# Optimization experiments

Hardware: AMD Instinct MI355X
Metric: run time of the kernel (lower is better)

The kernel has to match this reference:

```python
import jax, jax.numpy as jnp
import numpy as np

T = 4096
HIDDEN = 2048
N_HEADS = 16
N_KV_HEADS = 4
HEAD_DIM = 128
WINDOW = 1024  # per_layer_sliding_window = WINDOW + 1 -> q attends keys with q_pos - k_pos <= WINDOW
ROPE_THETA = 100000.0
QKV_OUT = (N_HEADS + 2 * N_KV_HEADS) * HEAD_DIM  # 3072


def setup_inputs() -> dict:
    key = jax.random.key(0)
    k1, k2, k3, k4 = jax.random.split(key, 4)
    return {
        "hidden_states": jax.random.normal(k1, (T, HIDDEN), dtype=jnp.float32),
        "positions": jnp.arange(T, dtype=jnp.int32),
        "w_qkv": jax.random.normal(k2, (HIDDEN, QKV_OUT), dtype=jnp.float32) * 0.02,
        "b_qkv": jax.random.normal(k3, (QKV_OUT,), dtype=jnp.float32) * 0.02,
        "w_o": jax.random.normal(k4, (N_HEADS * HEAD_DIM, HIDDEN), dtype=jnp.float32) * 0.02,
    }


def _apply_rope(x, positions):
    # x: [T, n_heads, HEAD_DIM], neox-style rotary over full head dim
    half = HEAD_DIM // 2
    inv_freq = 1.0 / (ROPE_THETA ** (jnp.arange(half, dtype=jnp.float32) / half))
    freqs = positions.astype(jnp.float32)[:, None] * inv_freq[None, :]  # [T, half]
    cos = jnp.cos(freqs)[:, None, :]  # [T, 1, half]
    sin = jnp.sin(freqs)[:, None, :]
    x1, x2 = x[..., :half], x[..., half:]
    return jnp.concatenate([x1 * cos - x2 * sin, x2 * cos + x1 * sin], axis=-1)


def reference(hidden_states, positions, w_qkv, b_qkv, w_o):
    # QKV projection (bias=True)
    qkv = hidden_states @ w_qkv + b_qkv  # [T, QKV_OUT]
    q_size = N_HEADS * HEAD_DIM
    kv_size = N_KV_HEADS * HEAD_DIM
    q = qkv[:, :q_size].reshape(T, N_HEADS, HEAD_DIM)
    k = qkv[:, q_size:q_size + kv_size].reshape(T, N_KV_HEADS, HEAD_DIM)
    v = qkv[:, q_size + kv_size:].reshape(T, N_KV_HEADS, HEAD_DIM)

    # RoPE on q and k
    q = _apply_rope(q, positions)
    k = _apply_rope(k, positions)

    # GQA: expand kv heads to match query heads
    group = N_HEADS // N_KV_HEADS
    k = jnp.repeat(k, group, axis=1)  # [T, N_HEADS, HEAD_DIM]
    v = jnp.repeat(v, group, axis=1)

    scale = HEAD_DIM ** -0.5
    scores = jnp.einsum('qhd,khd->hqk', q, k) * scale  # [H, T, T]

    # causal + sliding-window mask: j <= i and i - j <= WINDOW
    i = jnp.arange(T)[:, None]
    j = jnp.arange(T)[None, :]
    mask = (j <= i) & (i - j <= WINDOW)  # [T, T]
    scores = jnp.where(mask[None, :, :], scores, jnp.finfo(scores.dtype).min)

    probs = jax.nn.softmax(scores, axis=-1)
    attn = jnp.einsum('hqk,khd->qhd', probs, v)  # [T, H, HEAD_DIM]
    attn = attn.reshape(T, N_HEADS * HEAD_DIM)

    # output projection (bias=False)
    return attn @ w_o
```

## Files before the change

### kernel.cpp

```cpp
#include <hip/hip_runtime.h>
#include <cstdint>

#define T_TOK 4096
#define HID 2048
#define NH 16
#define NKV 4
#define HD 128
#define WIN 1024
#define QKVO 3072

typedef float f32x4 __attribute__((ext_vector_type(4)));
typedef __bf16 bf16x8 __attribute__((ext_vector_type(8)));
typedef __bf16 bf16x4 __attribute__((ext_vector_type(4)));
typedef __bf16 bf16x2 __attribute__((ext_vector_type(2)));

__device__ __forceinline__ void gload16(const void* g, void* lds) {
  auto gp = reinterpret_cast<__attribute__((address_space(1))) void*>(
      reinterpret_cast<uintptr_t>(g));
  auto lp = reinterpret_cast<__attribute__((address_space(3))) void*>(
      reinterpret_cast<uintptr_t>(lds));
  __builtin_amdgcn_global_load_lds(gp, lp, 16, 0, 0);
}

__device__ __forceinline__ f32x4 mfma16(bf16x8 a, bf16x8 b, f32x4 c) {
  return __builtin_amdgcn_mfma_f32_16x16x32_bf16(a, b, c, 0, 0, 0);
}

__global__ __launch_bounds__(256) void k_f32_to_bf16(const float* __restrict__ x,
                                                     __bf16* __restrict__ y) {
  const size_t e = (size_t)blockIdx.x * 256 + threadIdx.x;
  const float4* xv = (const float4*)x;
  float4 a = xv[e * 2], b = xv[e * 2 + 1];
  bf16x8 o;
  o[0] = (__bf16)a.x; o[1] = (__bf16)a.y; o[2] = (__bf16)a.z; o[3] = (__bf16)a.w;
  o[4] = (__bf16)b.x; o[5] = (__bf16)b.y; o[6] = (__bf16)b.z; o[7] = (__bf16)b.w;
  *(bf16x8*)(y + e * 8) = o;
}

__global__ __launch_bounds__(256) void k_transpose(const float* __restrict__ W,
                                                   __bf16* __restrict__ Wt,
                                                   int R, int C) {
  __shared__ __bf16 tb[32][33];
  const int nbx = C >> 5;
  const int c0 = (blockIdx.x % nbx) << 5;
  const int r0 = (blockIdx.x / nbx) << 5;
  const int tx = threadIdx.x & 31, ty = threadIdx.x >> 5;
#pragma unroll
  for (int i = 0; i < 32; i += 8)
    tb[ty + i][tx] = (__bf16)W[(size_t)(r0 + ty + i) * C + c0 + tx];
  __syncthreads();
#pragma unroll
  for (int i = 0; i < 32; i += 8)
    Wt[(size_t)(c0 + ty + i) * R + r0 + tx] = tb[tx][ty + i];
}

__global__ void k_rope_tab(const int* __restrict__ pos, float* __restrict__ cosT,
                           float* __restrict__ sinT) {
  const int t = blockIdx.x;
  const int d = threadIdx.x;
  const float inv = exp2f(-(float)d * (16.609640474436812f / 64.0f));
  const float fr = (float)pos[t] * inv;
  cosT[t * 64 + d] = cosf(fr);
  sinT[t * 64 + d] = sinf(fr);
}

template <bool BIAS, typename OutT>
__global__ __launch_bounds__(256, 2) void k_gemm(const __bf16* __restrict__ A,
                                                 const __bf16* __restrict__ Bt,
                                                 const float* __restrict__ bias,
                                                 OutT* __restrict__ C,
                                                 int M, int N, int K) {
  __shared__ __align__(16) __bf16 As[128 * 32];
  __shared__ __align__(16) __bf16 Bs[128 * 32];
  const int tid = threadIdx.x;
  const int lane = tid & 63;
  const int w = tid >> 6;
  const int wr = w >> 1, wc = w & 1;
  const int c = lane & 15, g = lane >> 4;

  const int nbx = N >> 7;
  const int bx = blockIdx.x % nbx;
  const int by = blockIdx.x / nbx;
  const int m0 = by << 7, n0 = bx << 7;

  const int o0 = w * 2048 + lane * 16;
  const int r0 = o0 >> 6, cb0 = o0 & 63;
  const int o1 = o0 + 1024;
  const int r1 = o1 >> 6, cb1 = o1 & 63;
  const __bf16* gA0 = A + (size_t)(m0 + r0) * K + (cb0 >> 1);
  const __bf16* gA1 = A + (size_t)(m0 + r1) * K + (cb1 >> 1);
  const __bf16* gB0 = Bt + (size_t)(n0 + r0) * K + (cb0 >> 1);
  const __bf16* gB1 = Bt + (size_t)(n0 + r1) * K + (cb1 >> 1);
  char* lA0 = (char*)As + w * 2048;
  char* lA1 = lA0 + 1024;
  char* lB0 = (char*)Bs + w * 2048;
  char* lB1 = lB0 + 1024;

  f32x4 acc[4][4] = {};

  for (int kt = 0; kt < K; kt += 32) {
    __syncthreads();
    gload16(gA0 + kt, lA0);
    gload16(gA1 + kt, lA1);
    gload16(gB0 + kt, lB0);
    gload16(gB1 + kt, lB1);
    __syncthreads();
    bf16x8 af[4], bfr[4];
#pragma unroll
    for (int mi = 0; mi < 4; mi++)
      af[mi] = *(const bf16x8*)(As + ((wr * 64 + mi * 16 + c) * 32 + g * 8));
#pragma unroll
    for (int ni = 0; ni < 4; ni++)
      bfr[ni] = *(const bf16x8*)(Bs + ((wc * 64 + ni * 16 + c) * 32 + g * 8));
#pragma unroll
    for (int mi = 0; mi < 4; mi++)
#pragma unroll
      for (int ni = 0; ni < 4; ni++)
        acc[mi][ni] = mfma16(af[mi], bfr[ni], acc[mi][ni]);
  }

#pragma unroll
  for (int ni = 0; ni < 4; ni++) {
    const int col = n0 + wc * 64 + ni * 16 + c;
    const float bv = BIAS ? bias[col] : 0.0f;
#pragma unroll
    for (int mi = 0; mi < 4; mi++)
#pragma unroll
      for (int r = 0; r < 4; r++) {
        const int row = m0 + wr * 64 + mi * 16 + 4 * g + r;
        C[(size_t)row * N + col] = (OutT)(acc[mi][ni][r] + bv);
      }
  }
}

__global__ __launch_bounds__(256) void k_rope_pack(
    const __bf16* __restrict__ qkv, const float* __restrict__ cosT,
    const float* __restrict__ sinT, __bf16* __restrict__ Qp,
    __bf16* __restrict__ Kp, __bf16* __restrict__ Vt) {
  const int t0 = blockIdx.x * 64;
  const int hh = blockIdx.y;
  const int tid = threadIdx.x;
  const int col0 = hh * HD;
  __shared__ __bf16 lt[64][136];
  if (hh < NH + NKV) {
    const bool isq = hh < NH;
    const float s = isq ? 0.08838834764831845f : 1.0f;
    __bf16* base = isq ? (Qp + (size_t)hh * T_TOK * HD)
                       : (Kp + (size_t)(hh - NH) * T_TOK * HD);
#pragma unroll
    for (int jj = 0; jj < 2; jj++) {
      const int e = jj * 256 + tid;
      const int tl = e >> 3, ch = e & 7;
      const int tt = t0 + tl;
      const bf16x8 x1 = *(const bf16x8*)(qkv + (size_t)tt * QKVO + col0 + ch * 8);
      const bf16x8 x2 = *(const bf16x8*)(qkv + (size_t)tt * QKVO + col0 + 64 + ch * 8);
      const float4 c0 = *(const float4*)(cosT + tt * 64 + ch * 8);
      const float4 c1 = *(const float4*)(cosT + tt * 64 + ch * 8 + 4);
      const float4 s0 = *(const float4*)(sinT + tt * 64 + ch * 8);
      const float4 s1 = *(const float4*)(sinT + tt * 64 + ch * 8 + 4);
      const float cs[8] = {c0.x, c0.y, c0.z, c0.w, c1.x, c1.y, c1.z, c1.w};
      const float sn[8] = {s0.x, s0.y, s0.z, s0.w, s1.x, s1.y, s1.z, s1.w};
      bf16x8 o1, o2;
#pragma unroll
      for (int i = 0; i < 8; i++) {
        const float a = (float)x1[i], b = (float)x2[i];
        o1[i] = (__bf16)((a * cs[i] - b * sn[i]) * s);
        o2[i] = (__bf16)((b * cs[i] + a * sn[i]) * s);
      }
      const int d2s = isq ? ch * 8 : ((ch * 8) ^ ((tt & 7) << 3));
      __bf16* dst = base + (size_t)tt * HD;
      *(bf16x8*)(dst + d2s) = o1;
      *(bf16x8*)(dst + 64 + d2s) = o2;
    }
  } else {
    const int kv = hh - (NH + NKV);
#pragma unroll
    for (int jj = 0; jj < 4; jj++) {
      const int e = jj * 256 + tid;
      const int tl = e >> 4, dc = e & 15;
      *(bf16x8*)&lt[tl][dc * 8] =
          *(const bf16x8*)(qkv + (size_t)(t0 + tl) * QKVO + col0 + dc * 8);
    }
    __syncthreads();
#pragma unroll
    for (int jj = 0; jj < 32; jj++) {
      const int e = jj * 256 + tid;
      const int d = e >> 6, tl = e & 63;
      Vt[((size_t)kv * HD + d) * T_TOK + t0 + (tl ^ ((d & 7) << 3))] = lt[tl][d];
    }
  }
}

__global__ __launch_bounds__(512, 4) void k_attn(const __bf16* __restrict__ Qp,
                                                 const __bf16* __restrict__ Kp,
                                                 const __bf16* __restrict__ Vt,
                                                 __bf16* __restrict__ attnO) {
  __shared__ __align__(16) __bf16 Ks[2][64 * 128];
  __shared__ __align__(16) __bf16 Vs[2][128 * 64];
  __shared__ __align__(16) __bf16 Ps[8][16 * 64];

  const int tid = threadIdx.x;
  const int lane = tid & 63;
  const int w = tid >> 6;
  const int c = lane & 15, g = lane >> 4;
  const int h = blockIdx.y;
  const int kvh = h >> 2;
  const int qb = (int)(gridDim.x - 1) - (int)blockIdx.x;
  const int q0 = qb * 128;
  const int i_row = q0 + w * 16 + c;
  const int swz = (c & 7) << 4;

  bf16x8 qf[4];
  {
    const __bf16* qbase = Qp + ((size_t)h * T_TOK + i_row) * HD;
#pragma unroll
    for (int ds = 0; ds < 4; ds++) qf[ds] = *(const bf16x8*)(qbase + ds * 32 + g * 8);
  }

  f32x4 ot[8] = {};
  float mrun = 0.0f, lrun = 0.0f;

  const int jstart = (q0 >= WIN) ? (q0 - WIN) : 0;
  const int niter = (q0 + 128 - jstart) >> 6;

  const char* Kg = (const char*)Kp + (size_t)kvh * T_TOK * HD * 2;
  const char* Vg = (const char*)Vt + (size_t)kvh * HD * T_TOK * 2;
  const char* kg0 = Kg + (size_t)(jstart + 8 * w + (lane >> 4)) * 256 + (lane & 15) * 16;
  const char* vg0 = Vg + (size_t)(16 * w + (lane >> 3)) * (T_TOK * 2) +
                    (size_t)jstart * 2 + (lane & 7) * 16;

#pragma unroll
  for (int q = 0; q < 2; q++)
    gload16(kg0 + q * 1024, (char*)&Ks[0][0] + w * 2048 + q * 1024);
#pragma unroll
  for (int q = 0; q < 2; q++)
    gload16(vg0 + (size_t)q * 8 * (T_TOK * 2), (char*)&Vs[0][0] + w * 2048 + q * 1024);

  char* pw = (char*)&Ps[w][0];
  int cur = 0;

  for (int it = 0; it < niter; ++it) {
    const int j0 = jstart + it * 64;
    __syncthreads();

    if (it + 1 < niter) {
      const char* kg = kg0 + (size_t)(it + 1) * 16384;
      const char* vg = vg0 + (size_t)(it + 1) * 128;
      char* kd = (char*)&Ks[cur ^ 1][0] + w * 2048;
      char* vd = (char*)&Vs[cur ^ 1][0] + w * 2048;
#pragma unroll
      for (int q = 0; q < 2; q++) gload16(kg + q * 1024, kd + q * 1024);
#pragma unroll
      for (int q = 0; q < 2; q++)
        gload16(vg + (size_t)q * 8 * (T_TOK * 2), vd + q * 1024);
    }

    const char* kb = (const char*)&Ks[cur][0];
    const char* vb = (const char*)&Vs[cur][0];

    f32x4 st[4] = {};
    __builtin_amdgcn_s_setprio(1);
#pragma unroll
    for (int t = 0; t < 4; t++)
#pragma unroll
      for (int ds = 0; ds < 4; ds++) {
        bf16x8 kf = *(const bf16x8*)(kb + (t * 16 + c) * 256 + ((ds * 64 + g * 16) ^ swz));
        st[t] = mfma16(kf, qf[ds], st[t]);
      }
    __builtin_amdgcn_s_setprio(0);

    float p[16];
    float cmax = -1e30f;
    const int jb = i_row - j0 - 4 * g;
#pragma unroll
    for (int t = 0; t < 4; t++)
#pragma unroll
      for (int r = 0; r < 4; r++) {
        float s = st[t][r];
        s = ((unsigned)(jb - 16 * t - r) <= WIN) ? s : -1e30f;
        p[t * 4 + r] = s;
        cmax = fmaxf(cmax, s);
      }
    cmax = fmaxf(cmax, __shfl_xor(cmax, 16));
    cmax = fmaxf(cmax, __shfl_xor(cmax, 32));

    if (!__all(cmax <= mrun + 8.0f)) {
      const float mn = fmaxf(mrun, cmax);
      const float alpha = __expf(mrun - mn);
      lrun *= alpha;
#pragma unroll
      for (int m = 0; m < 8; m++) ot[m] *= alpha;
      mrun = mn;
    }
    float rs = 0.0f;
#pragma unroll
    for (int x = 0; x < 16; x++) {
      const float e_ = __expf(p[x] - mrun);
      p[x] = e_;
      rs += e_;
    }
    rs += __shfl_xor(rs, 16);
    rs += __shfl_xor(rs, 32);
    lrun += rs;

#pragma unroll
    for (int t = 0; t < 4; t++) {
      bf16x4 pk;
      pk[0] = (__bf16)p[t * 4 + 0];
      pk[1] = (__bf16)p[t * 4 + 1];
      pk[2] = (__bf16)p[t * 4 + 2];
      pk[3] = (__bf16)p[t * 4 + 3];
      *(bf16x4*)(pw + c * 128 + ((t * 32 + g * 8) ^ swz)) = pk;
    }
    bf16x8 pf[2];
#pragma unroll
    for (int ks = 0; ks < 2; ks++)
      pf[ks] = *(const bf16x8*)(pw + c * 128 + ((ks * 64 + g * 16) ^ swz));

    __builtin_amdgcn_s_setprio(1);
#pragma unroll
    for (int m = 0; m < 8; m++)
#pragma unroll
      for (int ks = 0; ks < 2; ks++) {
        bf16x8 vf = *(const bf16x8*)(vb + (m * 16 + c) * 128 + ((ks * 64 + g * 16) ^ swz));
        ot[m] = mfma16(vf, pf[ks], ot[m]);
      }
    __builtin_amdgcn_s_setprio(0);

    cur ^= 1;
  }

  const float inv_l = 1.0f / lrun;
  __bf16* orow = attnO + (size_t)i_row * (NH * HD) + h * HD;
#pragma unroll
  for (int m = 0; m < 8; m++) {
    bf16x4 o4;
#pragma unroll
    for (int r = 0; r < 4; r++) o4[r] = (__bf16)(ot[m][r] * inv_l);
    *(bf16x4*)(orow + m * 16 + 4 * g) = o4;
  }
}

extern "C" void kernel_launch(void* const* d_in, const int* in_sizes, int n_in,
                              void* d_out, int out_size, void* d_ws, size_t ws_size,
                              hipStream_t stream) {
  (void)in_sizes; (void)n_in; (void)out_size; (void)ws_size;
  const float* hidden = (const float*)d_in[0];
  const int* positions = (const int*)d_in[1];
  const float* w_qkv = (const float*)d_in[2];
  const float* b_qkv = (const float*)d_in[3];
  const float* w_o = (const float*)d_in[4];
  float* out = (float*)d_out;

  char* ws = (char*)d_ws;
  __bf16* Hb = (__bf16*)ws;    ws += (size_t)T_TOK * HID * 2;
  __bf16* Wqkvt = (__bf16*)ws; ws += (size_t)QKVO * HID * 2;
  __bf16* Wot = (__bf16*)ws;   ws += (size_t)HID * HID * 2;
  float* cosT = (float*)ws;    ws += (size_t)T_TOK * 64 * 4;
  float* sinT = (float*)ws;    ws += (size_t)T_TOK * 64 * 4;
  __bf16* qkv = (__bf16*)ws;   ws += (size_t)T_TOK * QKVO * 2;
  __bf16* Qp = (__bf16*)ws;    ws += (size_t)NH * T_TOK * HD * 2;
  __bf16* Kp = (__bf16*)ws;    ws += (size_t)NKV * T_TOK * HD * 2;
  __bf16* Vt = (__bf16*)ws;    ws += (size_t)NKV * HD * T_TOK * 2;
  __bf16* attnb = (__bf16*)ws; ws += (size_t)T_TOK * NH * HD * 2;

  k_f32_to_bf16<<<T_TOK * HID / (256 * 8), 256, 0, stream>>>(hidden, Hb);
  k_transpose<<<(QKVO / 32) * (HID / 32), 256, 0, stream>>>(w_qkv, Wqkvt, HID, QKVO);
  k_transpose<<<(HID / 32) * (HID / 32), 256, 0, stream>>>(w_o, Wot, HID, HID);
  k_rope_tab<<<T_TOK, 64, 0, stream>>>(positions, cosT, sinT);
  k_gemm<true, __bf16><<<(T_TOK / 128) * (QKVO / 128), 256, 0, stream>>>(
      Hb, Wqkvt, b_qkv, qkv, T_TOK, QKVO, HID);
  k_rope_pack<<<dim3(T_TOK / 64, NH + 2 * NKV), 256, 0, stream>>>(
      qkv, cosT, sinT, Qp, Kp, Vt);
  k_attn<<<dim3(T_TOK / 128, NH), 512, 0, stream>>>(Qp, Kp, Vt, attnb);
  k_gemm<false, float><<<(T_TOK / 128) * (HID / 128), 256, 0, stream>>>(
      attnb, Wot, nullptr, out, T_TOK, HID, HID);
}
```

Baseline: 199.4 us.

## Double-buffer GEMM LDS tiles, swizzle LDS layout, and remap blocks across XCDs

New measurement: 190.9 us. 1.04x faster.

```diff
diff --git a/kernel.cpp b/kernel.cpp
--- a/kernel.cpp
+++ b/kernel.cpp
@@ -70,53 +70,75 @@
                                                  const float* __restrict__ bias,
                                                  OutT* __restrict__ C,
                                                  int M, int N, int K) {
-  __shared__ __align__(16) __bf16 As[128 * 32];
-  __shared__ __align__(16) __bf16 Bs[128 * 32];
+  __shared__ __align__(16) __bf16 As[2][128 * 32];
+  __shared__ __align__(16) __bf16 Bs[2][128 * 32];
   const int tid = threadIdx.x;
   const int lane = tid & 63;
   const int w = tid >> 6;
   const int wr = w >> 1, wc = w & 1;
   const int c = lane & 15, g = lane >> 4;
-
-  const int nbx = N >> 7;
-  const int bx = blockIdx.x % nbx;
-  const int by = blockIdx.x / nbx;
+  const int gsw = g ^ ((c >> 1) & 3);
+
+  const int nstc = N >> 9;
+  const int bid = blockIdx.x;
+  const int xcd = bid & 7;
+  const int j = bid >> 3;
+  const int spx = (int)(gridDim.x >> 7);
+  const int s = xcd * spx + (j >> 4);
+  const int q = j & 15;
+  const int by = (s / nstc) * 4 + (q >> 2);
+  const int bx = (s % nstc) * 4 + (q & 3);
   const int m0 = by << 7, n0 = bx << 7;
 
   const int o0 = w * 2048 + lane * 16;
-  const int r0 = o0 >> 6, cb0 = o0 & 63;
+  const int r0 = o0 >> 6;
+  const int g0 = (lane & 3) ^ ((r0 >> 1) & 3);
   const int o1 = o0 + 1024;
-  const int r1 = o1 >> 6, cb1 = o1 & 63;
-  const __bf16* gA0 = A + (size_t)(m0 + r0) * K + (cb0 >> 1);
-  const __bf16* gA1 = A + (size_t)(m0 + r1) * K + (cb1 >> 1);
-  const __bf16* gB0 = Bt + (size_t)(n0 + r0) * K + (cb0 >> 1);
-  const __bf16* gB1 = Bt + (size_t)(n0 + r1) * K + (cb1 >> 1);
-  char* lA0 = (char*)As + w * 2048;
-  char* lA1 = lA0 + 1024;
-  char* lB0 = (char*)Bs + w * 2048;
-  char* lB1 = lB0 + 1024;
+  const int r1 = o1 >> 6;
+  const int g1 = (lane & 3) ^ ((r1 >> 1) & 3);
+  const __bf16* gA0 = A + (size_t)(m0 + r0) * K + g0 * 8;
+  const __bf16* gA1 = A + (size_t)(m0 + r1) * K + g1 * 8;
+  const __bf16* gB0 = Bt + (size_t)(n0 + r0) * K + g0 * 8;
+  const __bf16* gB1 = Bt + (size_t)(n0 + r1) * K + g1 * 8;
 
   f32x4 acc[4][4] = {};
 
+  {
+    char* la = (char*)&As[0][0];
+    char* lb = (char*)&Bs[0][0];
+    gload16(gA0, la + o0);
+    gload16(gA1, la + o1);
+    gload16(gB0, lb + o0);
+    gload16(gB1, lb + o1);
+  }
+  __syncthreads();
+
+  int cur = 0;
   for (int kt = 0; kt < K; kt += 32) {
-    __syncthreads();
-    gload16(gA0 + kt, lA0);
-    gload16(gA1 + kt, lA1);
-    gload16(gB0 + kt, lB0);
-    gload16(gB1 + kt, lB1);
-    __syncthreads();
+    if (kt + 32 < K) {
+      char* la = (char*)&As[0][0] + (cur ^ 1) * 8192;
+      char* lb = (char*)&Bs[0][0] + (cur ^ 1) * 8192;
+      gload16(gA0 + kt + 32, la + o0);
+      gload16(gA1 + kt + 32, la + o1);
+      gload16(gB0 + kt + 32, lb + o0);
+      gload16(gB1 + kt + 32, lb + o1);
+    }
+    const __bf16* as = &As[0][0] + cur * 4096;
+    const __bf16* bs = &Bs[0][0] + cur * 4096;
     bf16x8 af[4], bfr[4];
 #pragma unroll
     for (int mi = 0; mi < 4; mi++)
-      af[mi] = *(const bf16x8*)(As + ((wr * 64 + mi * 16 + c) * 32 + g * 8));
+      af[mi] = *(const bf16x8*)(as + (wr * 64 + mi * 16 + c) * 32 + gsw * 8);
 #pragma unroll
     for (int ni = 0; ni < 4; ni++)
-      bfr[ni] = *(const bf16x8*)(Bs + ((wc * 64 + ni * 16 + c) * 32 + g * 8));
+      bfr[ni] = *(const bf16x8*)(bs + (wc * 64 + ni * 16 + c) * 32 + gsw * 8);
 #pragma unroll
     for (int mi = 0; mi < 4; mi++)
 #pragma unroll
       for (int ni = 0; ni < 4; ni++)
         acc[mi][ni] = mfma16(af[mi], bfr[ni], acc[mi][ni]);
+    __syncthreads();
+    cur ^= 1;
   }
 
 #pragma unroll
```
